# Kernel optimization log

Measured on AMD Instinct MI355X. Metric: run time of the kernel, lower is better.

The kernel has to match this reference:

```python
import jax, jax.numpy as jnp
from jax import lax
import numpy as np

B, L, V, CD, H, T = 256, 300, 20, 30, 128, 6
WN, WD = 48, 128
START, STOP = 4, 5
NEG = -10000.0
SLOPE = 0.01  # nn.LeakyReLU default
BN_EPS = 1e-5
HH = H // 2


def leaky(x):
    return jnp.where(x >= 0, x, SLOPE * x)


def lstm_scan(x, w_ih, w_hh, b_ih, b_hh):
    # x: [B, L, D] -> outputs [B, L, HH]; torch gate order i,f,g,o
    def step(carry, x_t):
        h, c = carry
        g = x_t @ w_ih.T + h @ w_hh.T + b_ih + b_hh
        i, f, gg, o = jnp.split(g, 4, axis=-1)
        c = jax.nn.sigmoid(f) * c + jax.nn.sigmoid(i) * jnp.tanh(gg)
        h = jax.nn.sigmoid(o) * jnp.tanh(c)
        return (h, c), h
    z = jnp.zeros((x.shape[0], HH), x.dtype)
    _, ys = lax.scan(step, (z, z), x.transpose(1, 0, 2))
    return ys.transpose(1, 0, 2)


def reverse_by_length(x, lengths):
    # per-sample reversal within valid length; padded positions -> 0
    t = jnp.arange(x.shape[1])
    idx = lengths[:, None] - 1 - t[None, :]
    valid = (idx >= 0)[:, :, None].astype(x.dtype)
    idx = jnp.clip(idx, 0, x.shape[1] - 1)
    return jnp.take_along_axis(x, idx[:, :, None], axis=1) * valid


def conv2d(x, w, b, stride):
    y = lax.conv_general_dilated(x, w, (stride, stride), ((1, 1), (1, 1)),
                                 dimension_numbers=('NCHW', 'OIHW', 'NCHW'))
    return y + b[None, :, None, None]


def maxpool2(x):
    return lax.reduce_window(x, -jnp.inf, lax.max, (1, 1, 2, 2), (1, 1, 2, 2), 'VALID')


def bn(x, s, b):
    # eval-mode BatchNorm2d folded to affine (running_mean=0, running_var=1)
    return x * s[None, :, None, None] + b[None, :, None, None]


def forward(words, emb, w_ih_f, w_hh_f, b_ih_f, b_hh_f, w_ih_b, w_hh_b, b_ih_b, b_hh_b,
            w_lin_lstm, b_lin_lstm, conv1_w, conv1_b, bn1_s, bn1_b, conv2_w, conv2_b,
            bn2_s, bn2_b, conv3_w, conv3_b, bn3_s, bn3_b, w_lin_cnn, b_lin_cnn,
            w1, b1, w2, b2, w_tag, b_tag, transitions, characters, tags, length):
    mask = (jnp.arange(L)[None, :] < length[:, None])  # [B, L]
    fmask = mask.astype(jnp.float32)
    # ---- BiLSTM over char embeddings (pack/pad semantics via masking) ----
    chars_vec = emb[characters]  # [B, L, CD]
    out_f = lstm_scan(chars_vec, w_ih_f, w_hh_f, b_ih_f, b_hh_f) * fmask[:, :, None]
    rev = reverse_by_length(chars_vec, length)
    out_b = reverse_by_length(lstm_scan(rev, w_ih_b, w_hh_b, b_ih_b, b_hh_b), length)
    lstm_out = jnp.concatenate([out_f, out_b], axis=-1)  # [B, L, H]
    lstm_mapping = leaky(lstm_out @ w_lin_lstm.T + b_lin_lstm)
    # ---- CNN over word features ----
    x = words.reshape(B, 1, WN, WD)
    x = maxpool2(leaky(bn(conv2d(x, conv1_w, conv1_b, 2), bn1_s, bn1_b)))  # [B,16,12,32]
    x = maxpool2(leaky(bn(conv2d(x, conv2_w, conv2_b, 1), bn2_s, bn2_b)))  # [B,32,6,16]
    x = maxpool2(leaky(bn(conv2d(x, conv3_w, conv3_b, 1), bn3_s, bn3_b)))  # [B,64,3,8]
    cnn_flat = x.reshape(B, H, 12)
    cnn_mapping = leaky(cnn_flat @ w_lin_cnn.T + b_lin_cnn).reshape(B, L, H)
    # ---- fusion MLP -> emissions ----
    cat = jnp.concatenate([lstm_mapping, cnn_mapping], axis=-1)  # [B, L, 2H]
    h1 = leaky(cat @ w1.T + b1)
    h2 = leaky(h1 @ w2.T + b2)
    logits = leaky(h2 @ w_tag.T + b_tag)  # [B, L, T]
    # ---- CRF real path score ----
    prev_tags = jnp.concatenate([jnp.full((B, 1), START, tags.dtype), tags[:, :-1]], axis=1)
    emit = jnp.take_along_axis(logits, tags[:, :, None], axis=2)[..., 0]
    trans = transitions[prev_tags, tags]
    last_tag = jnp.take_along_axis(tags, (length - 1)[:, None], axis=1)[:, 0]
    real = jnp.sum((emit + trans) * fmask, axis=1) + transitions[last_tag, STOP]
    # ---- CRF forward algorithm (alpha init = zeros, matching original quirk) ----
    def step(alpha, xs):
        logit_t, m_t = xs
        new = jax.nn.logsumexp(alpha[:, :, None] + transitions[None, :, :], axis=1) + logit_t
        return jnp.where(m_t[:, None], new, alpha), None
    alpha0 = jnp.zeros((B, T), logits.dtype)
    alphaL, _ = lax.scan(step, alpha0, (logits.transpose(1, 0, 2), mask.T))
    total = jax.nn.logsumexp(alphaL + transitions[:, STOP][None, :], axis=1)
    return jnp.sum(total - real)[None]  # shape [1], like the torch code


def setup_inputs():
    keys = iter(jax.random.split(jax.random.key(0), 64))
    def rn(shape, s=0.1):
        return jax.random.normal(next(keys), shape, jnp.float32) * s
    inp = {}
    inp['characters'] = jax.random.randint(next(keys), (B, L), 0, V, jnp.int32)
    inp['tags'] = jax.random.randint(next(keys), (B, L), 0, 4, jnp.int32)
    inp['length'] = jax.random.randint(next(keys), (B,), 1, L + 1, jnp.int32)
    inp['words'] = jax.random.normal(next(keys), (B, WN, WD), jnp.float32)
    inp['emb'] = rn((V, CD), 1.0)
    for d in ('f', 'b'):
        inp['w_ih_' + d] = rn((4 * HH, CD))
        inp['w_hh_' + d] = rn((4 * HH, HH))
        inp['b_ih_' + d] = rn((4 * HH,))
        inp['b_hh_' + d] = rn((4 * HH,))
    inp['w_lin_lstm'] = rn((H, H)); inp['b_lin_lstm'] = rn((H,))
    inp['conv1_w'] = rn((16, 1, 3, 3)); inp['conv1_b'] = rn((16,))
    inp['bn1_s'] = jnp.full((16,), 1.0 / np.sqrt(1.0 + BN_EPS), jnp.float32); inp['bn1_b'] = jnp.zeros((16,), jnp.float32)
    inp['conv2_w'] = rn((32, 16, 3, 3)); inp['conv2_b'] = rn((32,))
    inp['bn2_s'] = jnp.full((32,), 1.0 / np.sqrt(1.0 + BN_EPS), jnp.float32); inp['bn2_b'] = jnp.zeros((32,), jnp.float32)
    inp['conv3_w'] = rn((64, 32, 3, 3)); inp['conv3_b'] = rn((64,))
    inp['bn3_s'] = jnp.full((64,), 1.0 / np.sqrt(1.0 + BN_EPS), jnp.float32); inp['bn3_b'] = jnp.zeros((64,), jnp.float32)
    inp['w_lin_cnn'] = rn((L, 12)); inp['b_lin_cnn'] = rn((L,))
    inp['w1'] = rn((100, 2 * H)); inp['b1'] = rn((100,))
    inp['w2'] = rn((94, 100)); inp['b2'] = rn((94,))
    inp['w_tag'] = rn((T, 94)); inp['b_tag'] = rn((T,))
    tr = rn((T, T), 1.0)
    tr = tr.at[START, :].set(NEG)
    tr = tr.at[:, STOP].set(NEG)
    inp['transitions'] = tr
    return inp


def reference(characters, tags, length, words, emb, w_ih_f, w_hh_f, b_ih_f, b_hh_f,
              w_ih_b, w_hh_b, b_ih_b, b_hh_b, w_lin_lstm, b_lin_lstm,
              conv1_w, conv1_b, bn1_s, bn1_b, conv2_w, conv2_b, bn2_s, bn2_b,
              conv3_w, conv3_b, bn3_s, bn3_b, w_lin_cnn, b_lin_cnn,
              w1, b1, w2, b2, w_tag, b_tag, transitions):
    return forward(words, emb, w_ih_f, w_hh_f, b_ih_f, b_hh_f, w_ih_b, w_hh_b, b_ih_b, b_hh_b,
                   w_lin_lstm, b_lin_lstm, conv1_w, conv1_b, bn1_s, bn1_b, conv2_w, conv2_b,
                   bn2_s, bn2_b, conv3_w, conv3_b, bn3_s, bn3_b, w_lin_cnn, b_lin_cnn,
                   w1, b1, w2, b2, w_tag, b_tag, transitions, characters, tags, length)
```

## Files before the change

### kernel.cpp

```cpp
#include <hip/hip_runtime.h>
#include <math.h>

#define B 256
#define LQ 300
#define V 20
#define CD 30
#define H 128
#define HH 64
#define TT 6
#define WN 48
#define WD 128
#define SLOPE 0.01f
#define START 4
#define STOP 5

__device__ __forceinline__ float fsig(float x) { return 1.0f / (1.0f + __expf(-x)); }
__device__ __forceinline__ float ftanh(float x) {
    x = fminf(fmaxf(x, -15.f), 15.f);
    float e = __expf(2.f * x);
    return (e - 1.f) / (e + 1.f);
}
__device__ __forceinline__ float lrelu(float x) { return x >= 0.f ? x : SLOPE * x; }

__global__ __launch_bounds__(256) void k_lstm(
    const int* __restrict__ chars, const int* __restrict__ length,
    const float* __restrict__ emb,
    const float* __restrict__ wihf, const float* __restrict__ whhf,
    const float* __restrict__ bihf, const float* __restrict__ bhhf,
    const float* __restrict__ wihb, const float* __restrict__ whhb,
    const float* __restrict__ bihb, const float* __restrict__ bhhb,
    float* __restrict__ lstm_out)
{
    __shared__ __align__(16) float emb_s[V * CD];
    __shared__ __align__(16) float pre_s[V * 256];
    __shared__ __align__(16) float h_s[2][HH];
    __shared__ int chars_s[LQ];
    int tid = threadIdx.x;
    int b = blockIdx.x >> 1;
    bool fwd = (blockIdx.x & 1) == 0;
    int gate = tid & 3, unit = tid >> 2;
    int row = gate * HH + unit;
    const float* wih = fwd ? wihf : wihb;
    const float* whh = fwd ? whhf : whhb;
    const float* bih = fwd ? bihf : bihb;
    const float* bhh = fwd ? bhhf : bhhb;
    for (int i = tid; i < V * CD; i += 256) emb_s[i] = emb[i];
    for (int i = tid; i < LQ; i += 256) chars_s[i] = chars[b * LQ + i];
    float wh[HH];
#pragma unroll
    for (int k = 0; k < HH; k++) wh[k] = whh[row * HH + k];
    float wi[CD];
#pragma unroll
    for (int k = 0; k < CD; k++) wi[k] = wih[row * CD + k];
    float bias = bih[row] + bhh[row];
    if (tid < 2 * HH) h_s[tid >> 6][tid & 63] = 0.f;
    int len = length[b];
    __syncthreads();
    for (int v = 0; v < V; ++v) {
        float a0 = bias, a1 = 0.f;
        const float* ev = emb_s + v * CD;
#pragma unroll
        for (int k = 0; k < CD; k += 2) {
            a0 = fmaf(wi[k], ev[k], a0);
            a1 = fmaf(wi[k + 1], ev[k + 1], a1);
        }
        pre_s[v * 256 + tid] = a0 + a1;
    }
    __syncthreads();
    float c = 0.f;
    int hofs = fwd ? 0 : HH;
    int lane = tid & 63, qbase = lane & ~3;
    int src0 = fwd ? 0 : (len - 1);
    float accx = pre_s[chars_s[src0] * 256 + tid];
    for (int t = 0; t < len; ++t) {
        int buf = t & 1;
        float acc_cur = accx;
        if (t + 1 < len) {
            int srcn = fwd ? (t + 1) : (len - 2 - t);
            accx = pre_s[chars_s[srcn] * 256 + tid];
        }
        const float4* hp4 = (const float4*)h_s[buf];
        float a0 = acc_cur, a1 = 0.f, a2 = 0.f, a3 = 0.f;
#pragma unroll
        for (int k4 = 0; k4 < 16; k4++) {
            float4 hv4 = hp4[k4];
            a0 = fmaf(wh[4 * k4], hv4.x, a0);
            a1 = fmaf(wh[4 * k4 + 1], hv4.y, a1);
            a2 = fmaf(wh[4 * k4 + 2], hv4.z, a2);
            a3 = fmaf(wh[4 * k4 + 3], hv4.w, a3);
        }
        float x = (a0 + a1) + (a2 + a3);
        float y = (gate == 2) ? 2.f * x : x;
        float s = 1.f / (1.f + __expf(-y));
        float a = (gate == 2) ? (2.f * s - 1.f) : s;
        float gi = __shfl(a, qbase + 0);
        float gf = __shfl(a, qbase + 1);
        float gg = __shfl(a, qbase + 2);
        float go = __shfl(a, qbase + 3);
        c = gf * c + gi * gg;
        float hv = go * ftanh(c);
        if (gate == 0) {
            int src = fwd ? t : (len - 1 - t);
            h_s[1 - buf][unit] = hv;
            lstm_out[((size_t)b * LQ + src) * H + hofs + unit] = hv;
        }
        __syncthreads();
    }
}

__global__ __launch_bounds__(256) void k_lstm_map(
    const float* __restrict__ lstm_out, const int* __restrict__ length,
    const float* __restrict__ wl, const float* __restrict__ bl,
    float* __restrict__ cat)
{
    __shared__ __align__(16) float row_s[8][128];
    __shared__ float part_s[2][8][128];
    __shared__ float b_s[128];
    int tid = threadIdx.x;
    int b = blockIdx.x >> 1, half = blockIdx.x & 1;
    int h = tid & 127, kh = tid >> 7;
    float w[64];
#pragma unroll
    for (int k = 0; k < 64; k++) w[k] = wl[h * 128 + kh * 64 + k];
    if (tid < 128) b_s[tid] = bl[tid];
    int len = length[b];
    const float* src = lstm_out + (size_t)b * LQ * H;
    float* dst = cat + (size_t)b * LQ * 256;
    int nrows = (len - half + 1) >> 1;
    for (int base = 0; base < nrows; base += 8) {
        __syncthreads();
        for (int i = tid; i < 8 * 128; i += 256) {
            int ri = i >> 7, k = i & 127;
            int rr = base + ri;
            if (rr < nrows) row_s[ri][k] = src[(size_t)(half + 2 * rr) * H + k];
        }
        __syncthreads();
        float acc[8];
#pragma unroll
        for (int r = 0; r < 8; r++) acc[r] = 0.f;
#pragma unroll
        for (int k4 = 0; k4 < 16; k4++) {
#pragma unroll
            for (int r = 0; r < 8; r++) {
                float4 x = ((const float4*)(row_s[r] + kh * 64))[k4];
                acc[r] = fmaf(w[4 * k4], x.x, acc[r]);
                acc[r] = fmaf(w[4 * k4 + 1], x.y, acc[r]);
                acc[r] = fmaf(w[4 * k4 + 2], x.z, acc[r]);
                acc[r] = fmaf(w[4 * k4 + 3], x.w, acc[r]);
            }
        }
#pragma unroll
        for (int r = 0; r < 8; r++) part_s[kh][r][h] = acc[r];
        __syncthreads();
        for (int i = tid; i < 1024; i += 256) {
            int r = i >> 7, o = i & 127;
            int rr = base + r;
            if (rr < nrows)
                dst[(size_t)(half + 2 * rr) * 256 + o] =
                    lrelu(b_s[o] + part_s[0][r][o] + part_s[1][r][o]);
        }
    }
}

__global__ void k_conv1(const float* __restrict__ words,
                        const float* __restrict__ cw, const float* __restrict__ cb,
                        const float* __restrict__ bs, const float* __restrict__ bb,
                        float* __restrict__ p1)
{
    int idx = blockIdx.x * 256 + threadIdx.x;
    int px = idx & 31;
    int t1 = idx >> 5;
    int py = t1 % 12;
    int t2 = t1 / 12;
    int oc = t2 & 15;
    int b = t2 >> 4;
    float w[9];
#pragma unroll
    for (int k = 0; k < 9; k++) w[k] = cw[oc * 9 + k];
    float patch[5][5];
    int iy0 = 4 * py - 1, ix0 = 4 * px - 1;
#pragma unroll
    for (int r = 0; r < 5; r++)
#pragma unroll
        for (int cc = 0; cc < 5; cc++) {
            int iy = iy0 + r, ix = ix0 + cc;
            patch[r][cc] = (iy >= 0 && iy < WN && ix >= 0 && ix < WD)
                               ? words[((size_t)b * WN + iy) * WD + ix] : 0.f;
        }
    float bias = cb[oc], s = bs[oc], sb = bb[oc];
    float best = -1e30f;
#pragma unroll
    for (int dy = 0; dy < 2; dy++)
#pragma unroll
        for (int dx = 0; dx < 2; dx++) {
            float acc = bias;
#pragma unroll
            for (int ky = 0; ky < 3; ky++)
#pragma unroll
                for (int kx = 0; kx < 3; kx++)
                    acc = fmaf(w[ky * 3 + kx], patch[2 * dy + ky][2 * dx + kx], acc);
            best = fmaxf(best, lrelu(acc * s + sb));
        }
    p1[idx] = best;
}

__global__ __launch_bounds__(256) void k_conv2(
    const float* __restrict__ p1,
    const float* __restrict__ cw, const float* __restrict__ cb,
    const float* __restrict__ bs, const float* __restrict__ bb,
    float* __restrict__ p2)
{
    __shared__ float in_s[16 * 14 * 34];
    __shared__ float w_s[16 * 16 * 9];
    int tid = threadIdx.x;
    int b = blockIdx.x >> 1;
    int oh = (blockIdx.x & 1) << 4;
    for (int i = tid; i < 16 * 14 * 34; i += 256) in_s[i] = 0.f;
    for (int i = tid; i < 16 * 16 * 9; i += 256) w_s[i] = cw[oh * 16 * 9 + i];
    __syncthreads();
    for (int i = tid; i < 16 * 12 * 32; i += 256) {
        int ic = i / 384;
        int r = i - ic * 384;
        int iy = r >> 5, ix = r & 31;
        in_s[ic * 476 + (iy + 1) * 34 + ix + 1] = p1[b * 6144 + i];
    }
    __syncthreads();
    int ocl = tid >> 4;
    int l16 = tid & 15;
    float acc[6][4];
    float bias = cb[oh + ocl];
#pragma unroll
    for (int q = 0; q < 6; q++)
#pragma unroll
        for (int j = 0; j < 4; j++) acc[q][j] = bias;
    for (int ic = 0; ic < 16; ic++) {
        const float* wp = w_s + (ocl * 16 + ic) * 9;
        float w[9];
#pragma unroll
        for (int k = 0; k < 9; k++) w[k] = wp[k];
        const float* ip = in_s + ic * 476;
#pragma unroll
        for (int q = 0; q < 6; q++) {
            int sp = l16 + (q << 4);
            int py = sp >> 4, px = sp & 15;
            const float* pb = ip + (2 * py) * 34 + 2 * px;
            float patch[4][4];
#pragma unroll
            for (int r = 0; r < 4; r++)
#pragma unroll
                for (int cc = 0; cc < 4; cc++) patch[r][cc] = pb[r * 34 + cc];
#pragma unroll
            for (int dy = 0; dy < 2; dy++)
#pragma unroll
                for (int dx = 0; dx < 2; dx++) {
                    float a = 0.f;
#pragma unroll
                    for (int ky = 0; ky < 3; ky++)
#pragma unroll
                        for (int kx = 0; kx < 3; kx++)
                            a = fmaf(w[ky * 3 + kx], patch[dy + ky][dx + kx], a);
                    acc[q][dy * 2 + dx] += a;
                }
        }
    }
    float s = bs[oh + ocl], sb = bb[oh + ocl];
#pragma unroll
    for (int q = 0; q < 6; q++) {
        float best = -1e30f;
#pragma unroll
        for (int j = 0; j < 4; j++) best = fmaxf(best, lrelu(acc[q][j] * s + sb));
        int sp = l16 + (q << 4);
        p2[((size_t)b * 32 + oh + ocl) * 96 + sp] = best;
    }
}

__global__ __launch_bounds__(256) void k_conv3(
    const float* __restrict__ p2,
    const float* __restrict__ cw, const float* __restrict__ cb,
    const float* __restrict__ bs, const float* __restrict__ bb,
    float* __restrict__ p3)
{
    __shared__ float in_s[32 * 8 * 18];
    __shared__ float w_s[32 * 32 * 9];
    int tid = threadIdx.x;
    int b = blockIdx.x >> 1;
    int oh = (blockIdx.x & 1) << 5;
    for (int i = tid; i < 32 * 8 * 18; i += 256) in_s[i] = 0.f;
    for (int i = tid; i < 32 * 32 * 9; i += 256) w_s[i] = cw[oh * 32 * 9 + i];
    __syncthreads();
    for (int i = tid; i < 32 * 6 * 16; i += 256) {
        int ic = i / 96;
        int r = i - ic * 96;
        int iy = r >> 4, ix = r & 15;
        in_s[ic * 144 + (iy + 1) * 18 + ix + 1] = p2[b * 3072 + i];
    }
    __syncthreads();
    int ocl = tid >> 3;
    int l8 = tid & 7;
    float acc[3][4];
    float bias = cb[oh + ocl];
#pragma unroll
    for (int q = 0; q < 3; q++)
#pragma unroll
        for (int j = 0; j < 4; j++) acc[q][j] = bias;
    for (int ic = 0; ic < 32; ic++) {
        const float* wp = w_s + (ocl * 32 + ic) * 9;
        float w[9];
#pragma unroll
        for (int k = 0; k < 9; k++) w[k] = wp[k];
        const float* ip = in_s + ic * 144;
#pragma unroll
        for (int q = 0; q < 3; q++) {
            int sp = l8 + (q << 3);
            int py = sp >> 3, px = sp & 7;
            const float* pb = ip + (2 * py) * 18 + 2 * px;
            float patch[4][4];
#pragma unroll
            for (int r = 0; r < 4; r++)
#pragma unroll
                for (int cc = 0; cc < 4; cc++) patch[r][cc] = pb[r * 18 + cc];
#pragma unroll
            for (int dy = 0; dy < 2; dy++)
#pragma unroll
                for (int dx = 0; dx < 2; dx++) {
                    float a = 0.f;
#pragma unroll
                    for (int ky = 0; ky < 3; ky++)
#pragma unroll
                        for (int kx = 0; kx < 3; kx++)
                            a = fmaf(w[ky * 3 + kx], patch[dy + ky][dx + kx], a);
                    acc[q][dy * 2 + dx] += a;
                }
        }
    }
    float s = bs[oh + ocl], sb = bb[oh + ocl];
#pragma unroll
    for (int q = 0; q < 3; q++) {
        float best = -1e30f;
#pragma unroll
        for (int j = 0; j < 4; j++) best = fmaxf(best, lrelu(acc[q][j] * s + sb));
        int sp = l8 + (q << 3);
        p3[((size_t)b * 64 + oh + ocl) * 24 + sp] = best;
    }
}

__global__ __launch_bounds__(256) void k_cnn_map(
    const float* __restrict__ p3, const int* __restrict__ length,
    const float* __restrict__ wlc, const float* __restrict__ blc,
    float* __restrict__ cat)
{
    __shared__ float flat_s[1536];
    __shared__ float w_s[3600];
    __shared__ float b_s[300];
    int tid = threadIdx.x, b = blockIdx.x;
    for (int i = tid; i < 1536; i += 256) flat_s[i] = p3[b * 1536 + i];
    for (int i = tid; i < 3600; i += 256) w_s[i] = wlc[i];
    for (int i = tid; i < 300; i += 256) b_s[i] = blc[i];
    int len = length[b];
    __syncthreads();
    int bound = len * 128;
    for (int j = tid; j < bound; j += 256) {
        int l = j >> 7, h = j & 127;
        int row = j / 300, col = j - row * 300;
        float acc = b_s[col];
#pragma unroll
        for (int k = 0; k < 12; k++) acc = fmaf(flat_s[row * 12 + k], w_s[col * 12 + k], acc);
        cat[((size_t)b * LQ + l) * 256 + H + h] = lrelu(acc);
    }
}

__global__ __launch_bounds__(512) void k_h1(
    const float* __restrict__ cat, const int* __restrict__ length,
    const float* __restrict__ w1, const float* __restrict__ b1,
    float* __restrict__ h1b)
{
    __shared__ __align__(16) float row_s[8][256];
    __shared__ float part_s[4][8][104];
    __shared__ float b_s[100];
    int tid = threadIdx.x;
    int b = blockIdx.x >> 1, half = blockIdx.x & 1;
    int lane = tid & 127, q = tid >> 7;
    bool act = lane < 100;
    float w[64];
    if (act) {
#pragma unroll
        for (int k = 0; k < 64; k++) w[k] = w1[lane * 256 + q * 64 + k];
    }
    if (tid < 100) b_s[tid] = b1[tid];
    int len = length[b];
    const float* src = cat + (size_t)b * LQ * 256;
    float* dst = h1b + (size_t)b * LQ * 100;
    int nrows = (len - half + 1) >> 1;
    for (int base = 0; base < nrows; base += 8) {
        __syncthreads();
        for (int i = tid; i < 8 * 256; i += 512) {
            int ri = i >> 8, k = i & 255;
            int rr = base + ri;
            if (rr < nrows) row_s[ri][k] = src[(size_t)(half + 2 * rr) * 256 + k];
        }
        __syncthreads();
        if (act) {
            float acc[8];
#pragma unroll
            for (int r = 0; r < 8; r++) acc[r] = 0.f;
#pragma unroll
            for (int k4 = 0; k4 < 16; k4++) {
#pragma unroll
                for (int r = 0; r < 8; r++) {
                    float4 x = ((const float4*)(row_s[r] + q * 64))[k4];
                    acc[r] = fmaf(w[4 * k4], x.x, acc[r]);
                    acc[r] = fmaf(w[4 * k4 + 1], x.y, acc[r]);
                    acc[r] = fmaf(w[4 * k4 + 2], x.z, acc[r]);
                    acc[r] = fmaf(w[4 * k4 + 3], x.w, acc[r]);
                }
            }
#pragma unroll
            for (int r = 0; r < 8; r++) part_s[q][r][lane] = acc[r];
        }
        __syncthreads();
        for (int i = tid; i < 800; i += 512) {
            int r = i / 100, o = i - r * 100;
            int rr = base + r;
            if (rr < nrows)
                dst[(size_t)(half + 2 * rr) * 100 + o] =
                    lrelu(b_s[o] + (part_s[0][r][o] + part_s[1][r][o]) +
                          (part_s[2][r][o] + part_s[3][r][o]));
        }
    }
}

__global__ __launch_bounds__(256) void k_h2_logits(
    const float* __restrict__ h1b, const int* __restrict__ length,
    const float* __restrict__ w2, const float* __restrict__ b2,
    const float* __restrict__ wt, const float* __restrict__ bt,
    float* __restrict__ logits)
{
    __shared__ __align__(16) float row_s[8][104];
    __shared__ float part_s[2][8][96];
    __shared__ float h2_s[8][96];
    __shared__ float wt_s[6 * 94];
    __shared__ float bt_s[6];
    __shared__ float b2_s[94];
    int tid = threadIdx.x;
    int b = blockIdx.x >> 1, half = blockIdx.x & 1;
    int o = tid & 127, kh = tid >> 7;
    bool act = o < 94;
    int kbase = kh * 52;
    float w[52];
    if (act) {
#pragma unroll
        for (int k = 0; k < 52; k++)
            w[k] = (kbase + k < 100) ? w2[o * 100 + kbase + k] : 0.f;
    }
    if (tid < 94) b2_s[tid] = b2[tid];
    for (int i = tid; i < 564; i += 256) wt_s[i] = wt[i];
    if (tid < 6) bt_s[tid] = bt[tid];
    int len = length[b];
    const float* src = h1b + (size_t)b * LQ * 100;
    float* dst = logits + (size_t)b * LQ * TT;
    int nrows = (len - half + 1) >> 1;
    for (int base = 0; base < nrows; base += 8) {
        __syncthreads();
        for (int i = tid; i < 8 * 104; i += 256) {
            int r = i / 104, k = i - r * 104;
            int rr = base + r;
            row_s[r][k] = (k < 100 && rr < nrows) ? src[(size_t)(half + 2 * rr) * 100 + k] : 0.f;
        }
        __syncthreads();
        if (act) {
            float acc[8];
#pragma unroll
            for (int r = 0; r < 8; r++) acc[r] = 0.f;
#pragma unroll
            for (int k4 = 0; k4 < 13; k4++) {
#pragma unroll
                for (int r = 0; r < 8; r++) {
                    float4 x = ((const float4*)(row_s[r] + kbase))[k4];
                    acc[r] = fmaf(w[4 * k4], x.x, acc[r]);
                    acc[r] = fmaf(w[4 * k4 + 1], x.y, acc[r]);
                    acc[r] = fmaf(w[4 * k4 + 2], x.z, acc[r]);
                    acc[r] = fmaf(w[4 * k4 + 3], x.w, acc[r]);
                }
            }
#pragma unroll
            for (int r = 0; r < 8; r++) part_s[kh][r][o] = acc[r];
        }
        __syncthreads();
        for (int i = tid; i < 752; i += 256) {
            int r = i / 94, oo = i - r * 94;
            h2_s[r][oo] = lrelu(b2_s[oo] + part_s[0][r][oo] + part_s[1][r][oo]);
        }
        __syncthreads();
        if (tid < 48) {
            int r = tid / 6, tag = tid - r * 6;
            int rr = base + r;
            if (rr < nrows) {
                float a0 = bt_s[tag], a1 = 0.f;
#pragma unroll
                for (int k = 0; k < 94; k += 2) {
                    a0 = fmaf(wt_s[tag * 94 + k], h2_s[r][k], a0);
                    a1 = fmaf(wt_s[tag * 94 + k + 1], h2_s[r][k + 1], a1);
                }
                dst[(size_t)(half + 2 * rr) * TT + tag] = lrelu(a0 + a1);
            }
        }
    }
}

__global__ __launch_bounds__(64) void k_crf(
    const float* __restrict__ logits, const int* __restrict__ tags,
    const int* __restrict__ length, const float* __restrict__ trans,
    float* __restrict__ crfv)
{
    int tid = threadIdx.x, b = blockIdx.x;
    int len = length[b];
    const int* tg = tags + b * LQ;
    float s = 0.f;
    for (int t = tid; t < len; t += 64) {
        int cur = tg[t];
        int prev = (t == 0) ? START : tg[t - 1];
        s += logits[((size_t)b * LQ + t) * TT + cur] + trans[prev * TT + cur];
    }
#pragma unroll
    for (int off = 32; off > 0; off >>= 1) s += __shfl_down(s, off);
    float real = __shfl(s, 0) + trans[tg[len - 1] * TT + STOP];
    int j = (tid < TT) ? tid : 0;
    float trc[TT];
#pragma unroll
    for (int i = 0; i < TT; i++) trc[i] = trans[i * TT + j];
    float tstop = trans[j * TT + STOP];
    float alpha = 0.f;
    for (int t = 0; t < len; ++t) {
        float lg = logits[((size_t)b * LQ + t) * TT + j];
        float a0 = __shfl(alpha, 0), a1 = __shfl(alpha, 1), a2 = __shfl(alpha, 2);
        float a3 = __shfl(alpha, 3), a4 = __shfl(alpha, 4), a5 = __shfl(alpha, 5);
        float v0 = a0 + trc[0], v1 = a1 + trc[1], v2 = a2 + trc[2];
        float v3 = a3 + trc[3], v4 = a4 + trc[4], v5 = a5 + trc[5];
        float m = fmaxf(fmaxf(fmaxf(v0, v1), fmaxf(v2, v3)), fmaxf(v4, v5));
        float sum = __expf(v0 - m) + __expf(v1 - m) + __expf(v2 - m) +
                    __expf(v3 - m) + __expf(v4 - m) + __expf(v5 - m);
        alpha = m + __logf(sum) + lg;
    }
    float v = alpha + tstop;
    float w0 = __shfl(v, 0), w1 = __shfl(v, 1), w2 = __shfl(v, 2);
    float w3 = __shfl(v, 3), w4 = __shfl(v, 4), w5 = __shfl(v, 5);
    float m2 = fmaxf(fmaxf(fmaxf(w0, w1), fmaxf(w2, w3)), fmaxf(w4, w5));
    float total = m2 + __logf(__expf(w0 - m2) + __expf(w1 - m2) + __expf(w2 - m2) +
                              __expf(w3 - m2) + __expf(w4 - m2) + __expf(w5 - m2));
    if (tid == 0) crfv[b] = total - real;
}

__global__ void k_sum(const float* __restrict__ crfv, float* __restrict__ out)
{
    __shared__ float red[4];
    int tid = threadIdx.x;
    float v = crfv[tid];
#pragma unroll
    for (int off = 32; off > 0; off >>= 1) v += __shfl_down(v, off);
    if ((tid & 63) == 0) red[tid >> 6] = v;
    __syncthreads();
    if (tid == 0) out[0] = red[0] + red[1] + red[2] + red[3];
}

extern "C" void kernel_launch(void* const* d_in, const int* in_sizes, int n_in,
                              void* d_out, int out_size, void* d_ws, size_t ws_size,
                              hipStream_t stream)
{
    const int* characters = (const int*)d_in[0];
    const int* tags       = (const int*)d_in[1];
    const int* length     = (const int*)d_in[2];
    const float* words    = (const float*)d_in[3];
    const float* emb      = (const float*)d_in[4];
    const float* w_ih_f   = (const float*)d_in[5];
    const float* w_hh_f   = (const float*)d_in[6];
    const float* b_ih_f   = (const float*)d_in[7];
    const float* b_hh_f   = (const float*)d_in[8];
    const float* w_ih_b   = (const float*)d_in[9];
    const float* w_hh_b   = (const float*)d_in[10];
    const float* b_ih_b   = (const float*)d_in[11];
    const float* b_hh_b   = (const float*)d_in[12];
    const float* w_lin_lstm = (const float*)d_in[13];
    const float* b_lin_lstm = (const float*)d_in[14];
    const float* conv1_w  = (const float*)d_in[15];
    const float* conv1_b  = (const float*)d_in[16];
    const float* bn1_s    = (const float*)d_in[17];
    const float* bn1_b    = (const float*)d_in[18];
    const float* conv2_w  = (const float*)d_in[19];
    const float* conv2_b  = (const float*)d_in[20];
    const float* bn2_s    = (const float*)d_in[21];
    const float* bn2_b    = (const float*)d_in[22];
    const float* conv3_w  = (const float*)d_in[23];
    const float* conv3_b  = (const float*)d_in[24];
    const float* bn3_s    = (const float*)d_in[25];
    const float* bn3_b    = (const float*)d_in[26];
    const float* w_lin_cnn = (const float*)d_in[27];
    const float* b_lin_cnn = (const float*)d_in[28];
    const float* w1       = (const float*)d_in[29];
    const float* b1       = (const float*)d_in[30];
    const float* w2       = (const float*)d_in[31];
    const float* b2       = (const float*)d_in[32];
    const float* w_tag    = (const float*)d_in[33];
    const float* b_tag    = (const float*)d_in[34];
    const float* trans    = (const float*)d_in[35];

    float* ws = (float*)d_ws;
    float* lstm_out = ws;
    float* cat      = lstm_out + (size_t)B * LQ * H;
    float* p1       = cat + (size_t)B * LQ * 256;
    float* p2       = p1 + (size_t)B * 16 * 12 * 32;
    float* p3       = p2 + (size_t)B * 32 * 6 * 16;
    float* logits   = p3 + (size_t)B * 1536;
    float* crfv     = logits + (size_t)B * LQ * TT;
    float* h1b      = lstm_out;

    k_lstm<<<512, 256, 0, stream>>>(characters, length, emb,
                                    w_ih_f, w_hh_f, b_ih_f, b_hh_f,
                                    w_ih_b, w_hh_b, b_ih_b, b_hh_b, lstm_out);
    k_conv1<<<6144, 256, 0, stream>>>(words, conv1_w, conv1_b, bn1_s, bn1_b, p1);
    k_conv2<<<512, 256, 0, stream>>>(p1, conv2_w, conv2_b, bn2_s, bn2_b, p2);
    k_conv3<<<512, 256, 0, stream>>>(p2, conv3_w, conv3_b, bn3_s, bn3_b, p3);
    k_lstm_map<<<512, 256, 0, stream>>>(lstm_out, length, w_lin_lstm, b_lin_lstm, cat);
    k_cnn_map<<<256, 256, 0, stream>>>(p3, length, w_lin_cnn, b_lin_cnn, cat);
    k_h1<<<512, 512, 0, stream>>>(cat, length, w1, b1, h1b);
    k_h2_logits<<<512, 256, 0, stream>>>(h1b, length, w2, b2, w_tag, b_tag, logits);
    k_crf<<<256, 64, 0, stream>>>(logits, tags, length, trans, crfv);
    k_sum<<<1, 256, 0, stream>>>(crfv, (float*)d_out);
}
```

Baseline: 768.2 us.

## Split LSTM recurrent dot product across quad lanes by input chunk

Changes the LSTM thread mapping so each of four lanes per hidden unit computes all four gates over a 16-element slice of h, then reduces the partial sums with xor shuffles. Previously each lane owned one gate and did a full 64-wide dot product followed by four gather shuffles. The aim is to shorten the serial FMA dependency chain per timestep and let every lane compute the nonlinearities redundantly instead of shuffling gate values. It adds two shuffle rounds per gate and redundant transcendental work, and the precompute table now stores float4 per unit.

```diff
diff --git a/kernel.cpp b/kernel.cpp
--- a/kernel.cpp
+++ b/kernel.cpp
@@ -32,74 +32,101 @@
     float* __restrict__ lstm_out)
 {
     __shared__ __align__(16) float emb_s[V * CD];
-    __shared__ __align__(16) float pre_s[V * 256];
+    __shared__ __align__(16) float pre_s[V * HH * 4];
     __shared__ __align__(16) float h_s[2][HH];
     __shared__ int chars_s[LQ];
     int tid = threadIdx.x;
     int b = blockIdx.x >> 1;
     bool fwd = (blockIdx.x & 1) == 0;
-    int gate = tid & 3, unit = tid >> 2;
-    int row = gate * HH + unit;
+    int unit = tid >> 2, q = tid & 3;
     const float* wih = fwd ? wihf : wihb;
     const float* whh = fwd ? whhf : whhb;
     const float* bih = fwd ? bihf : bihb;
     const float* bhh = fwd ? bhhf : bhhb;
     for (int i = tid; i < V * CD; i += 256) emb_s[i] = emb[i];
     for (int i = tid; i < LQ; i += 256) chars_s[i] = chars[b * LQ + i];
-    float wh[HH];
-#pragma unroll
-    for (int k = 0; k < HH; k++) wh[k] = whh[row * HH + k];
-    float wi[CD];
-#pragma unroll
-    for (int k = 0; k < CD; k++) wi[k] = wih[row * CD + k];
-    float bias = bih[row] + bhh[row];
+    float w[4][16];
+#pragma unroll
+    for (int g = 0; g < 4; g++)
+#pragma unroll
+        for (int k = 0; k < 16; k++)
+            w[g][k] = whh[(g * HH + unit) * HH + q * 16 + k];
+    float wiq[4][8];
+#pragma unroll
+    for (int g = 0; g < 4; g++)
+#pragma unroll
+        for (int k = 0; k < 8; k++) {
+            int kk = q * 8 + k;
+            wiq[g][k] = (kk < CD) ? wih[(g * HH + unit) * CD + kk] : 0.f;
+        }
+    float bvec[4];
+#pragma unroll
+    for (int g = 0; g < 4; g++)
+        bvec[g] = (q == 0) ? (bih[g * HH + unit] + bhh[g * HH + unit]) : 0.f;
     if (tid < 2 * HH) h_s[tid >> 6][tid & 63] = 0.f;
     int len = length[b];
     __syncthreads();
     for (int v = 0; v < V; ++v) {
-        float a0 = bias, a1 = 0.f;
         const float* ev = emb_s + v * CD;
-#pragma unroll
-        for (int k = 0; k < CD; k += 2) {
-            a0 = fmaf(wi[k], ev[k], a0);
-            a1 = fmaf(wi[k + 1], ev[k + 1], a1);
-        }
-        pre_s[v * 256 + tid] = a0 + a1;
+        float p[4];
+#pragma unroll
+        for (int g = 0; g < 4; g++) {
+            float a = bvec[g];
+#pragma unroll
+            for (int k = 0; k < 8; k++) {
+                int kk = q * 8 + k;
+                float x = (kk < CD) ? ev[kk] : 0.f;
+                a = fmaf(wiq[g][k], x, a);
+            }
+            p[g] = a;
+        }
+#pragma unroll
+        for (int g = 0; g < 4; g++) {
+            p[g] += __shfl_xor(p[g], 1);
+            p[g] += __shfl_xor(p[g], 2);
+        }
+        if (q == 0) {
+            float4 pv = make_float4(p[0], p[1], p[2], p[3]);
+            *(float4*)&pre_s[(v * HH + unit) * 4] = pv;
+        }
     }
     __syncthreads();
     float c = 0.f;
     int hofs = fwd ? 0 : HH;
-    int lane = tid & 63, qbase = lane & ~3;
     int src0 = fwd ? 0 : (len - 1);
-    float accx = pre_s[chars_s[src0] * 256 + tid];
+    float4 accx = *(const float4*)&pre_s[(chars_s[src0] * HH + unit) * 4];
     for (int t = 0; t < len; ++t) {
         int buf = t & 1;
-        float acc_cur = accx;
+        float4 pcur = accx;
         if (t + 1 < len) {
             int srcn = fwd ? (t + 1) : (len - 2 - t);
-            accx = pre_s[chars_s[srcn] * 256 + tid];
-        }
-        const float4* hp4 = (const float4*)h_s[buf];
-        float a0 = acc_cur, a1 = 0.f, a2 = 0.f, a3 = 0.f;
-#pragma unroll
-        for (int k4 = 0; k4 < 16; k4++) {
-            float4 hv4 = hp4[k4];
-            a0 = fmaf(wh[4 * k4], hv4.x, a0);
-            a1 = fmaf(wh[4 * k4 + 1], hv4.y, a1);
-            a2 = fmaf(wh[4 * k4 + 2], hv4.z, a2);
-            a3 = fmaf(wh[4 * k4 + 3], hv4.w, a3);
-        }
-        float x = (a0 + a1) + (a2 + a3);
-        float y = (gate == 2) ? 2.f * x : x;
-        float s = 1.f / (1.f + __expf(-y));
-        float a = (gate == 2) ? (2.f * s - 1.f) : s;
-        float gi = __shfl(a, qbase + 0);
-        float gf = __shfl(a, qbase + 1);
-        float gg = __shfl(a, qbase + 2);
-        float go = __shfl(a, qbase + 3);
+            accx = *(const float4*)&pre_s[(chars_s[srcn] * HH + unit) * 4];
+        }
+        const float4* hp4 = (const float4*)&h_s[buf][q * 16];
+        float a[4] = {0.f, 0.f, 0.f, 0.f};
+#pragma unroll
+        for (int j = 0; j < 4; j++) {
+            float4 hv4 = hp4[j];
+#pragma unroll
+            for (int g = 0; g < 4; g++) {
+                a[g] = fmaf(w[g][4 * j], hv4.x, a[g]);
+                a[g] = fmaf(w[g][4 * j + 1], hv4.y, a[g]);
+                a[g] = fmaf(w[g][4 * j + 2], hv4.z, a[g]);
+                a[g] = fmaf(w[g][4 * j + 3], hv4.w, a[g]);
+            }
+        }
+#pragma unroll
+        for (int g = 0; g < 4; g++) {
+            a[g] += __shfl_xor(a[g], 1);
+            a[g] += __shfl_xor(a[g], 2);
+        }
+        float gi = fsig(pcur.x + a[0]);
+        float gf = fsig(pcur.y + a[1]);
+        float gg = ftanh(pcur.z + a[2]);
+        float go = fsig(pcur.w + a[3]);
         c = gf * c + gi * gg;
         float hv = go * ftanh(c);
-        if (gate == 0) {
+        if (q == 0) {
             int src = fwd ? t : (len - 1 - t);
             h_s[1 - buf][unit] = hv;
             lstm_out[((size_t)b * LQ + src) * H + hofs + unit] = hv;
```

Result: slower. 786.5 us (+2.4%).

## Compute all four LSTM gates per thread in a single-wavefront block

Applied to the files above, without the earlier changes.

Restructures the LSTM recurrence so each of 64 threads owns one hidden unit and computes all four gate dot products, holding 256 recurrent weights in registers. This removes the four cross-lane shuffles per step and turns the per-step barrier into one within a single wavefront, which should be cheap. The trade is four times the serial FMA work per thread, very high register pressure (about 256+ VGPRs), and only 64-thread blocks. The input projection table is also stored gate-interleaved, so one float4 load fetches all four gate pre-activations.

```diff
diff --git a/kernel.cpp b/kernel.cpp
--- a/kernel.cpp
+++ b/kernel.cpp
@@ -22,7 +22,7 @@
 }
 __device__ __forceinline__ float lrelu(float x) { return x >= 0.f ? x : SLOPE * x; }
 
-__global__ __launch_bounds__(256) void k_lstm(
+__global__ __launch_bounds__(64) void k_lstm(
     const int* __restrict__ chars, const int* __restrict__ length,
     const float* __restrict__ emb,
     const float* __restrict__ wihf, const float* __restrict__ whhf,
@@ -32,78 +32,92 @@
     float* __restrict__ lstm_out)
 {
     __shared__ __align__(16) float emb_s[V * CD];
-    __shared__ __align__(16) float pre_s[V * 256];
+    __shared__ __align__(16) float pre_s[V * HH * 4];
     __shared__ __align__(16) float h_s[2][HH];
     __shared__ int chars_s[LQ];
-    int tid = threadIdx.x;
+    int unit = threadIdx.x;
     int b = blockIdx.x >> 1;
     bool fwd = (blockIdx.x & 1) == 0;
-    int gate = tid & 3, unit = tid >> 2;
-    int row = gate * HH + unit;
     const float* wih = fwd ? wihf : wihb;
     const float* whh = fwd ? whhf : whhb;
     const float* bih = fwd ? bihf : bihb;
     const float* bhh = fwd ? bhhf : bhhb;
-    for (int i = tid; i < V * CD; i += 256) emb_s[i] = emb[i];
-    for (int i = tid; i < LQ; i += 256) chars_s[i] = chars[b * LQ + i];
-    float wh[HH];
-#pragma unroll
-    for (int k = 0; k < HH; k++) wh[k] = whh[row * HH + k];
-    float wi[CD];
-#pragma unroll
-    for (int k = 0; k < CD; k++) wi[k] = wih[row * CD + k];
-    float bias = bih[row] + bhh[row];
-    if (tid < 2 * HH) h_s[tid >> 6][tid & 63] = 0.f;
+    for (int i = unit; i < V * CD; i += 64) emb_s[i] = emb[i];
+    for (int i = unit; i < LQ; i += 64) chars_s[i] = chars[b * LQ + i];
+    float bvec[4];
+#pragma unroll
+    for (int g = 0; g < 4; g++) bvec[g] = bih[g * HH + unit] + bhh[g * HH + unit];
+    h_s[0][unit] = 0.f;
     int len = length[b];
     __syncthreads();
-    for (int v = 0; v < V; ++v) {
-        float a0 = bias, a1 = 0.f;
-        const float* ev = emb_s + v * CD;
-#pragma unroll
-        for (int k = 0; k < CD; k += 2) {
-            a0 = fmaf(wi[k], ev[k], a0);
-            a1 = fmaf(wi[k + 1], ev[k + 1], a1);
-        }
-        pre_s[v * 256 + tid] = a0 + a1;
-    }
+    {
+        float wiq[4][CD];
+#pragma unroll
+        for (int g = 0; g < 4; g++)
+#pragma unroll
+            for (int k = 0; k < CD; k++) wiq[g][k] = wih[(g * HH + unit) * CD + k];
+        for (int v = 0; v < V; ++v) {
+            const float* ev = emb_s + v * CD;
+            float a[4] = {bvec[0], bvec[1], bvec[2], bvec[3]};
+#pragma unroll
+            for (int k = 0; k < CD; k++) {
+                float x = ev[k];
+#pragma unroll
+                for (int g = 0; g < 4; g++) a[g] = fmaf(wiq[g][k], x, a[g]);
+            }
+            *(float4*)&pre_s[(v * HH + unit) * 4] = make_float4(a[0], a[1], a[2], a[3]);
+        }
+    }
+    asm volatile("" ::: "memory");
+    float4 w4[4][16];
+#pragma unroll
+    for (int g = 0; g < 4; g++)
+#pragma unroll
+        for (int k4 = 0; k4 < 16; k4++)
+            w4[g][k4] = *(const float4*)&whh[(g * HH + unit) * HH + k4 * 4];
     __syncthreads();
     float c = 0.f;
     int hofs = fwd ? 0 : HH;
-    int lane = tid & 63, qbase = lane & ~3;
     int src0 = fwd ? 0 : (len - 1);
-    float accx = pre_s[chars_s[src0] * 256 + tid];
+    float4 pre = *(const float4*)&pre_s[(chars_s[src0] * HH + unit) * 4];
     for (int t = 0; t < len; ++t) {
         int buf = t & 1;
-        float acc_cur = accx;
+        float4 pcur = pre;
         if (t + 1 < len) {
             int srcn = fwd ? (t + 1) : (len - 2 - t);
-            accx = pre_s[chars_s[srcn] * 256 + tid];
+            pre = *(const float4*)&pre_s[(chars_s[srcn] * HH + unit) * 4];
         }
         const float4* hp4 = (const float4*)h_s[buf];
-        float a0 = acc_cur, a1 = 0.f, a2 = 0.f, a3 = 0.f;
+        float a0 = 0.f, a1 = 0.f, a2 = 0.f, a3 = 0.f;
 #pragma unroll
         for (int k4 = 0; k4 < 16; k4++) {
-            float4 hv4 = hp4[k4];
-            a0 = fmaf(wh[4 * k4], hv4.x, a0);
-            a1 = fmaf(wh[4 * k4 + 1], hv4.y, a1);
-            a2 = fmaf(wh[4 * k4 + 2], hv4.z, a2);
-            a3 = fmaf(wh[4 * k4 + 3], hv4.w, a3);
-        }
-        float x = (a0 + a1) + (a2 + a3);
-        float y = (gate == 2) ? 2.f * x : x;
-        float s = 1.f / (1.f + __expf(-y));
-        float a = (gate == 2) ? (2.f * s - 1.f) : s;
-        float gi = __shfl(a, qbase + 0);
-        float gf = __shfl(a, qbase + 1);
-        float gg = __shfl(a, qbase + 2);
-        float go = __shfl(a, qbase + 3);
+            float4 hv = hp4[k4];
+            a0 = fmaf(w4[0][k4].x, hv.x, a0);
+            a0 = fmaf(w4[0][k4].y, hv.y, a0);
+            a0 = fmaf(w4[0][k4].z, hv.z, a0);
+            a0 = fmaf(w4[0][k4].w, hv.w, a0);
+            a1 = fmaf(w4[1][k4].x, hv.x, a1);
+            a1 = fmaf(w4[1][k4].y, hv.y, a1);
+            a1 = fmaf(w4[1][k4].z, hv.z, a1);
+            a1 = fmaf(w4[1][k4].w, hv.w, a1);
+            a2 = fmaf(w4[2][k4].x, hv.x, a2);
+            a2 = fmaf(w4[2][k4].y, hv.y, a2);
+            a2 = fmaf(w4[2][k4].z, hv.z, a2);
+            a2 = fmaf(w4[2][k4].w, hv.w, a2);
+            a3 = fmaf(w4[3][k4].x, hv.x, a3);
+            a3 = fmaf(w4[3][k4].y, hv.y, a3);
+            a3 = fmaf(w4[3][k4].z, hv.z, a3);
+            a3 = fmaf(w4[3][k4].w, hv.w, a3);
+        }
+        float gi = fsig(pcur.x + a0);
+        float gf = fsig(pcur.y + a1);
+        float gg = ftanh(pcur.z + a2);
+        float go = fsig(pcur.w + a3);
         c = gf * c + gi * gg;
         float hv = go * ftanh(c);
-        if (gate == 0) {
-            int src = fwd ? t : (len - 1 - t);
-            h_s[1 - buf][unit] = hv;
-            lstm_out[((size_t)b * LQ + src) * H + hofs + unit] = hv;
-        }
+        int srcw = fwd ? t : (len - 1 - t);
+        h_s[1 - buf][unit] = hv;
+        lstm_out[((size_t)b * LQ + srcw) * H + hofs + unit] = hv;
         __syncthreads();
     }
 }
@@ -613,9 +627,9 @@
     float* crfv     = logits + (size_t)B * LQ * TT;
     float* h1b      = lstm_out;
 
-    k_lstm<<<512, 256, 0, stream>>>(characters, length, emb,
-                                    w_ih_f, w_hh_f, b_ih_f, b_hh_f,
-                                    w_ih_b, w_hh_b, b_ih_b, b_hh_b, lstm_out);
+    k_lstm<<<512, 64, 0, stream>>>(characters, length, emb,
+                                   w_ih_f, w_hh_f, b_ih_f, b_hh_f,
+                                   w_ih_b, w_hh_b, b_ih_b, b_hh_b, lstm_out);
     k_conv1<<<6144, 256, 0, stream>>>(words, conv1_w, conv1_b, bn1_s, bn1_b, p1);
     k_conv2<<<512, 256, 0, stream>>>(p1, conv2_w, conv2_b, bn2_s, bn2_b, p2);
     k_conv3<<<512, 256, 0, stream>>>(p2, conv3_w, conv3_b, bn3_s, bn3_b, p3);
```

After: 947.0 us. 23.3% more time.
